# Kernel optimization log

Measured on AMD Instinct MI355X. Metric: run time of the kernel, lower is better.

The kernel has to match this reference:

```python
import jax, jax.numpy as jnp
import numpy as np
import math

BLKQ = 64
BLKK = 32
TOPK_FRAC = 0.1


def setup_inputs() -> dict:
    key = jax.random.key(0)
    k1, k2, k3, k4, k5 = jax.random.split(key, 5)
    B, L, H, D = 1, 8192, 16, 64
    q = jax.random.normal(k1, (B, L, H, D), jnp.float32)
    k = jax.random.normal(k2, (B, L, H, D), jnp.float32)
    v = jax.random.normal(k3, (B, L, H, D), jnp.float32)
    # proj_l initialized with nn.init.normal_ (std=1) in the original
    W_proj = jax.random.normal(k4, (D, D), jnp.float32)
    b_proj = jax.random.normal(k5, (D,), jnp.float32)
    return {"q": q, "k": k, "v": v, "W_proj": W_proj, "b_proj": b_proj}


def reference(q, k, v, W_proj, b_proj):
    B, L, H, D = q.shape
    lcm = BLKQ * BLKK // math.gcd(BLKQ, BLKK)
    L_pad = ((L + lcm - 1) // lcm) * lcm
    pad = L_pad - L
    scale = 1.0 / math.sqrt(D)

    # [B, L, H, D] -> [B, H, L_pad, D], zero padded (fused_transpose_pad)
    qt = jnp.transpose(q, (0, 2, 1, 3))
    kt = jnp.transpose(k, (0, 2, 1, 3))
    vt = jnp.transpose(v, (0, 2, 1, 3))
    if pad:
        pw = ((0, 0), (0, 0), (0, pad), (0, 0))
        qt_p = jnp.pad(qt, pw); kt_p = jnp.pad(kt, pw); vt_p = jnp.pad(vt, pw)
    else:
        qt_p, kt_p, vt_p = qt, kt, vt

    # key smoothing (SAGE): subtract per-(b,h) mean of padded k
    km = kt_p.mean(axis=-2, keepdims=True)          # [B, H, 1, D]
    kc = kt_p - km

    M = L_pad // BLKQ
    N = L_pad // BLKK
    # block pooling for routing scores
    pooled_q = qt_p.reshape(B, H, M, BLKQ, D).mean(axis=3)   # [B,H,M,D]
    pooled_k = kc.reshape(B, H, N, BLKK, D).mean(axis=3)     # [B,H,N,D]
    score = jnp.einsum('bhmd,bhnd->bhmn', pooled_q, pooled_k)

    T = min(N, int(TOPK_FRAC * N))                  # real_topk (static)
    _, idx = jax.lax.top_k(score, T)                # [B,H,M,T]
    lut = jnp.sort(idx, axis=-1)

    # gather selected key/value blocks: [B,H,M,T,BLKK,D]
    kb = kc.reshape(B, H, N, BLKK, D)
    vb = vt_p.reshape(B, H, N, BLKK, D)
    kg = jnp.take_along_axis(kb[:, :, None], lut[..., None, None], axis=3)
    vg = jnp.take_along_axis(vb[:, :, None], lut[..., None, None], axis=3)

    qb = qt_p.reshape(B, H, M, BLKQ, D)
    # block-sparse scores: [B,H,M,BLKQ,T,BLKK]
    s = jnp.einsum('bhmqd,bhmtkd->bhmqtk', qb, kg) * scale
    key_pos = lut[..., None] * BLKK + jnp.arange(BLKK)       # [B,H,M,T,BLKK]
    valid = key_pos < L
    s = jnp.where(valid[:, :, :, None, :, :], s, -jnp.inf)
    s = s.reshape(B, H, M, BLKQ, T * BLKK)
    p = jax.nn.softmax(s, axis=-1)
    o_s = jnp.einsum('bhmqn,bhmnd->bhmqd', p, vg.reshape(B, H, M, T * BLKK, D))
    o_s = o_s.reshape(B, H, L_pad, D)[:, :, :L]              # slice to seq_len

    # linear attention branch (softmax feature map over D)
    q_fm = jax.nn.softmax(qt_p[:, :, :L], axis=-1)
    k_fm = jax.nn.softmax(kt_p[:, :, :L], axis=-1)
    kvsum = jnp.einsum('bhld,bhle->bhde', k_fm, vt)          # [B,H,D,D]
    ksum = k_fm.sum(axis=-2)                                 # [B,H,D]
    denom = jnp.einsum('bhld,bhd->bhl', q_fm, ksum)[..., None] + 1e-6
    o_l = jnp.einsum('bhld,bhde->bhle', q_fm, kvsum) / denom
    o_l = o_l @ W_proj.T + b_proj                            # proj_l

    o = jnp.transpose(o_l + o_s, (0, 2, 1, 3))               # [B,L,H,D]
    return o
```

## Files before the change

### kernel.cpp

```cpp
#include <hip/hip_runtime.h>
#include <math.h>

#define SEQL 8192
#define NH 16
#define HD 1024
#define TSEL 25

#define OFF_KVPART 0
#define OFF_KSUM   262144
#define OFF_ZEND   263168
#define OFF_PK     263168
#define OFF_KWT    525312
#define OFF_KSWZ   558080
#define OFF_LUT    131072

typedef __attribute__((ext_vector_type(8))) short bf16x8;
typedef __attribute__((ext_vector_type(4))) float f32x4;
typedef __attribute__((ext_vector_type(4))) unsigned u32x4;
typedef __attribute__((ext_vector_type(2))) unsigned u32x2;

static __device__ inline short f2bf(float f) {
    union { float f; unsigned u; } c; c.f = f;
    unsigned r = (c.u + 0x7FFFu + ((c.u >> 16) & 1u)) >> 16;
    return (short)r;
}
static __device__ inline bf16x8 cvt8(float4 a, float4 b) {
    bf16x8 r;
    r[0] = f2bf(a.x); r[1] = f2bf(a.y); r[2] = f2bf(a.z); r[3] = f2bf(a.w);
    r[4] = f2bf(b.x); r[5] = f2bf(b.y); r[6] = f2bf(b.z); r[7] = f2bf(b.w);
    return r;
}
static __device__ inline unsigned cvtpk(float a, float b) {
    unsigned r;
    asm("v_cvt_pk_bf16_f32 %0, %1, %2" : "=v"(r) : "v"(a), "v"(b));
    return r;
}
static __device__ inline float exp2a(float x) {
#if __has_builtin(__builtin_amdgcn_exp2f)
    return __builtin_amdgcn_exp2f(x);
#else
    float r; asm("v_exp_f32 %0, %1" : "=v"(r) : "v"(x)); return r;
#endif
}
#if __has_builtin(__builtin_amdgcn_permlane32_swap)
static __device__ inline unsigned xor32v(unsigned x, bool hi) {
    u32x2 r;
    {
        auto t = __builtin_amdgcn_permlane32_swap(x, x, false, false);
        r[0] = t[0]; r[1] = t[1];
    }
    return hi ? r[0] : r[1];
}
static __device__ inline unsigned xor16v(unsigned x, bool hi) {
    u32x2 r;
    {
        auto t = __builtin_amdgcn_permlane16_swap(x, x, false, false);
        r[0] = t[0]; r[1] = t[1];
    }
    return hi ? r[0] : r[1];
}
#else
static __device__ inline unsigned xor32v(unsigned x, bool hi) {
    unsigned a = x, b;
    asm("v_mov_b32 %0, %1" : "=v"(b) : "v"(x));
    asm("v_permlane32_swap_b32 %0, %1" : "+v"(a), "+v"(b));
    return hi ? a : b;
}
static __device__ inline unsigned xor16v(unsigned x, bool hi) {
    unsigned a = x, b;
    asm("v_mov_b32 %0, %1" : "=v"(b) : "v"(x));
    asm("v_permlane16_swap_b32 %0, %1" : "+v"(a), "+v"(b));
    return hi ? a : b;
}
#endif
static __device__ inline void load_lds16(const void* g, void* l) {
    __builtin_amdgcn_global_load_lds((const __attribute__((address_space(1))) unsigned int*)g,
                                     (__attribute__((address_space(3))) unsigned int*)l,
                                     16, 0, 0);
}

__global__ __launch_bounds__(256) void prep_lin(const float* __restrict__ k,
                                                const float* __restrict__ v,
                                                short* __restrict__ kswz,
                                                short* __restrict__ vswz,
                                                float* __restrict__ pk,
                                                float* __restrict__ kvpart,
                                                float* __restrict__ ksum) {
    __shared__ __align__(16) float kf[2][64][68];
    __shared__ __align__(16) float vv[2][64][68];
    __shared__ float pcol[2][2][4][64];
    int b = blockIdx.x;
    int h = b >> 5, sc = b & 31;
    int t = threadIdx.x;
    int lane = t & 63, w = t >> 6;
    int r32 = t >> 3, ch = t & 7;
    int d0 = (lane >> 4) * 4 + w * 16;
    int e0 = (lane & 15) * 4;
    float acc[16];
    #pragma unroll
    for (int i = 0; i < 16; i++) acc[i] = 0.f;
    float ks_acc = 0.f;

    const float* kb_ = k + (size_t)(sc * 256 + r32) * HD + h * 64 + ch * 8;
    const float* vb_ = v + (size_t)(sc * 256 + r32) * HD + h * 64 + ch * 8;
    float4 K0a = *(const float4*)kb_;
    float4 K0b = *(const float4*)(kb_ + 4);
    float4 K1a = *(const float4*)(kb_ + (size_t)32 * HD);
    float4 K1b = *(const float4*)(kb_ + (size_t)32 * HD + 4);
    float4 V0a = *(const float4*)vb_;
    float4 V0b = *(const float4*)(vb_ + 4);
    float4 V1a = *(const float4*)(vb_ + (size_t)32 * HD);
    float4 V1b = *(const float4*)(vb_ + (size_t)32 * HD + 4);

    #pragma unroll
    for (int ph = 0; ph < 4; ph++) {
        int buf = ph & 1;
        int n0 = sc * 8 + ph * 2;
        {
            *(float4*)&vv[buf][r32][ch * 8]          = V0a;
            *(float4*)&vv[buf][r32][ch * 8 + 4]      = V0b;
            *(float4*)&vv[buf][32 + r32][ch * 8]     = V1a;
            *(float4*)&vv[buf][32 + r32][ch * 8 + 4] = V1b;
        }
        {
            int f = r32 * 8 + (ch ^ (r32 & 7));
            *(bf16x8*)(kswz + (size_t)(h * 256 + n0) * 2048 + f * 8)     = cvt8(K0a, K0b);
            *(bf16x8*)(kswz + (size_t)(h * 256 + n0 + 1) * 2048 + f * 8) = cvt8(K1a, K1b);
        }
        {
            float s_[8] = { K0a.x, K0a.y, K0a.z, K0a.w, K0b.x, K0b.y, K0b.z, K0b.w };
            #pragma unroll
            for (int j = 0; j < 8; j++) {
                s_[j] += __shfl_xor(s_[j], 8, 64);
                s_[j] += __shfl_xor(s_[j], 16, 64);
                s_[j] += __shfl_xor(s_[j], 32, 64);
            }
            if (lane < 8) {
                #pragma unroll
                for (int j = 0; j < 8; j++) pcol[buf][0][w][(t & 7) * 8 + j] = s_[j];
            }
            float s1_[8] = { K1a.x, K1a.y, K1a.z, K1a.w, K1b.x, K1b.y, K1b.z, K1b.w };
            #pragma unroll
            for (int j = 0; j < 8; j++) {
                s1_[j] += __shfl_xor(s1_[j], 8, 64);
                s1_[j] += __shfl_xor(s1_[j], 16, 64);
                s1_[j] += __shfl_xor(s1_[j], 32, 64);
            }
            if (lane < 8) {
                #pragma unroll
                for (int j = 0; j < 8; j++) pcol[buf][1][w][(t & 7) * 8 + j] = s1_[j];
            }
        }
        {
            float mx = fmaxf(fmaxf(fmaxf(K0a.x, K0a.y), fmaxf(K0a.z, K0a.w)),
                             fmaxf(fmaxf(K0b.x, K0b.y), fmaxf(K0b.z, K0b.w)));
            mx = fmaxf(mx, __shfl_xor(mx, 1, 64));
            mx = fmaxf(mx, __shfl_xor(mx, 2, 64));
            mx = fmaxf(mx, __shfl_xor(mx, 4, 64));
            float4 Fa, Fb;
            Fa.x = __expf(K0a.x - mx); Fa.y = __expf(K0a.y - mx);
            Fa.z = __expf(K0a.z - mx); Fa.w = __expf(K0a.w - mx);
            Fb.x = __expf(K0b.x - mx); Fb.y = __expf(K0b.y - mx);
            Fb.z = __expf(K0b.z - mx); Fb.w = __expf(K0b.w - mx);
            float sm = (Fa.x + Fa.y + Fa.z + Fa.w) + (Fb.x + Fb.y + Fb.z + Fb.w);
            sm += __shfl_xor(sm, 1, 64);
            sm += __shfl_xor(sm, 2, 64);
            sm += __shfl_xor(sm, 4, 64);
            float inv = 1.f / sm;
            Fa.x *= inv; Fa.y *= inv; Fa.z *= inv; Fa.w *= inv;
            Fb.x *= inv; Fb.y *= inv; Fb.z *= inv; Fb.w *= inv;
            *(float4*)&kf[buf][r32][ch * 8]     = Fa;
            *(float4*)&kf[buf][r32][ch * 8 + 4] = Fb;
        }
        {
            float mx = fmaxf(fmaxf(fmaxf(K1a.x, K1a.y), fmaxf(K1a.z, K1a.w)),
                             fmaxf(fmaxf(K1b.x, K1b.y), fmaxf(K1b.z, K1b.w)));
            mx = fmaxf(mx, __shfl_xor(mx, 1, 64));
            mx = fmaxf(mx, __shfl_xor(mx, 2, 64));
            mx = fmaxf(mx, __shfl_xor(mx, 4, 64));
            float4 Fa, Fb;
            Fa.x = __expf(K1a.x - mx); Fa.y = __expf(K1a.y - mx);
            Fa.z = __expf(K1a.z - mx); Fa.w = __expf(K1a.w - mx);
            Fb.x = __expf(K1b.x - mx); Fb.y = __expf(K1b.y - mx);
            Fb.z = __expf(K1b.z - mx); Fb.w = __expf(K1b.w - mx);
            float sm = (Fa.x + Fa.y + Fa.z + Fa.w) + (Fb.x + Fb.y + Fb.z + Fb.w);
            sm += __shfl_xor(sm, 1, 64);
            sm += __shfl_xor(sm, 2, 64);
            sm += __shfl_xor(sm, 4, 64);
            float inv = 1.f / sm;
            Fa.x *= inv; Fa.y *= inv; Fa.z *= inv; Fa.w *= inv;
            Fb.x *= inv; Fb.y *= inv; Fb.z *= inv; Fb.w *= inv;
            *(float4*)&kf[buf][32 + r32][ch * 8]     = Fa;
            *(float4*)&kf[buf][32 + r32][ch * 8 + 4] = Fb;
        }
        if (ph < 3) {
            const float* kn = kb_ + (size_t)(ph + 1) * 64 * HD;
            const float* vn = vb_ + (size_t)(ph + 1) * 64 * HD;
            K0a = *(const float4*)kn;
            K0b = *(const float4*)(kn + 4);
            K1a = *(const float4*)(kn + (size_t)32 * HD);
            K1b = *(const float4*)(kn + (size_t)32 * HD + 4);
            V0a = *(const float4*)vn;
            V0b = *(const float4*)(vn + 4);
            V1a = *(const float4*)(vn + (size_t)32 * HD);
            V1b = *(const float4*)(vn + (size_t)32 * HD + 4);
        }
        __syncthreads();
        if (t < 128) {
            int s = t >> 6, d = t & 63;
            pk[(size_t)(h * 256 + n0 + s) * 64 + d] =
                (pcol[buf][s][0][d] + pcol[buf][s][1][d] + pcol[buf][s][2][d] + pcol[buf][s][3][d])
                * (1.f / 32.f);
        }
        {
            int c = w, d = lane;
            #pragma unroll
            for (int s = 0; s < 2; s++) {
                bf16x8 val;
                #pragma unroll
                for (int j = 0; j < 8; j++) val[j] = f2bf(vv[buf][s * 32 + c * 8 + j][d]);
                int f = d * 4 + (c ^ ((d >> 1) & 3));
                *(bf16x8*)(vswz + (size_t)(h * 256 + n0 + s) * 2048 + f * 8) = val;
            }
        }
        #pragma unroll 8
        for (int l = 0; l < 64; l++) {
            float4 kd = *(const float4*)&kf[buf][l][d0];
            float4 ve = *(const float4*)&vv[buf][l][e0];
            acc[0]  += kd.x * ve.x; acc[1]  += kd.x * ve.y; acc[2]  += kd.x * ve.z; acc[3]  += kd.x * ve.w;
            acc[4]  += kd.y * ve.x; acc[5]  += kd.y * ve.y; acc[6]  += kd.y * ve.z; acc[7]  += kd.y * ve.w;
            acc[8]  += kd.z * ve.x; acc[9]  += kd.z * ve.y; acc[10] += kd.z * ve.z; acc[11] += kd.z * ve.w;
            acc[12] += kd.w * ve.x; acc[13] += kd.w * ve.y; acc[14] += kd.w * ve.z; acc[15] += kd.w * ve.w;
        }
        if (t < 64) {
            float s = 0.f;
            #pragma unroll 8
            for (int l = 0; l < 64; l++) s += kf[buf][l][t];
            ks_acc += s;
        }
    }
    float* dst = kvpart + ((size_t)(sc & 3) * 16 + h) * 4096;
    #pragma unroll
    for (int i = 0; i < 4; i++)
        #pragma unroll
        for (int j = 0; j < 4; j++)
            atomicAdd(&dst[(d0 + i) * 64 + e0 + j], acc[i * 4 + j]);
    if (t < 64) atomicAdd(&ksum[h * 64 + t], ks_acc);
}

__global__ __launch_bounds__(256) void score_topk(const float* __restrict__ q,
                                                  const float* __restrict__ pk,
                                                  int* __restrict__ lut) {
    __shared__ __align__(16) float pq_s[64];
    __shared__ __align__(16) float s_s[256];
    __shared__ int wcnt[4];
    int b = blockIdx.x;
    int h = b >> 7, m = b & 127;
    int t = threadIdx.x;
    int lane = t & 63, w = t >> 6;
    if (t < 64) {
        const float* base = q + (size_t)m * 64 * HD + h * 64 + t;
        float s = 0.f;
        #pragma unroll 8
        for (int r = 0; r < 64; r++) s += base[(size_t)r * HD];
        pq_s[t] = s * (1.f / 64.f);
    }
    __syncthreads();
    const float* kr = pk + ((size_t)h * 256 + t) * 64;
    double acc = 0.0;
    #pragma unroll 8
    for (int d = 0; d < 64; d++) acc += (double)pq_s[d] * (double)kr[d];
    float sc = (float)acc;
    s_s[t] = sc;
    __syncthreads();
    int cnt = 0;
    float si = sc;
    #pragma unroll 4
    for (int j4 = 0; j4 < 64; j4++) {
        float4 sv = *(const float4*)&s_s[j4 * 4];
        int j = j4 * 4;
        cnt += (sv.x > si) || (sv.x == si && (j + 0) < t);
        cnt += (sv.y > si) || (sv.y == si && (j + 1) < t);
        cnt += (sv.z > si) || (sv.z == si && (j + 2) < t);
        cnt += (sv.w > si) || (sv.w == si && (j + 3) < t);
    }
    bool sel = cnt < TSEL;
    unsigned long long bal = __ballot(sel);
    if (lane == 0) wcnt[w] = __popcll(bal);
    __syncthreads();
    if (sel) {
        int off = __popcll(bal & ((1ull << lane) - 1ull));
        for (int i = 0; i < w; i++) off += wcnt[i];
        lut[(size_t)b * TSEL + off] = t;
    }
}

__global__ __launch_bounds__(256) void kw_mul(const float* __restrict__ kvpart,
                                              const float* __restrict__ W,
                                              short* __restrict__ kwt) {
    __shared__ __align__(16) float kv[16][68];
    __shared__ __align__(16) float wsm[64][68];
    int h = blockIdx.x >> 2, dq = blockIdx.x & 3;
    int t = threadIdx.x;
    for (int i = t; i < 1024; i += 256) {
        int dl = i >> 6, e = i & 63;
        float s = 0.f;
        #pragma unroll
        for (int p = 0; p < 4; p++)
            s += kvpart[((size_t)p * 16 + h) * 4096 + (dq * 16 + dl) * 64 + e];
        kv[dl][e] = s;
    }
    for (int i = t; i < 4096; i += 256) wsm[i >> 6][i & 63] = W[i];
    __syncthreads();
    int lane = t & 63, wi = t >> 6;
    int dl = lane & 15;
    int db = wi * 16 + (lane >> 4) * 4;
    #pragma unroll
    for (int j = 0; j < 4; j++) {
        int dd = db + j;
        float a = 0.f;
        #pragma unroll
        for (int e4 = 0; e4 < 16; e4++) {
            float4 kq = *(const float4*)&kv[dl][e4 * 4];
            float4 wq = *(const float4*)&wsm[dd][e4 * 4];
            a += kq.x * wq.x + kq.y * wq.y + kq.z * wq.z + kq.w * wq.w;
        }
        kwt[(size_t)h * 4096 + dd * 64 + dq * 16 + dl] = f2bf(a);
    }
}

__global__ __launch_bounds__(256) void sparse_attn_mfma(const float* __restrict__ q,
                                                        const short* __restrict__ kswz,
                                                        const short* __restrict__ vswz,
                                                        const int* __restrict__ lut,
                                                        const short* __restrict__ kwt,
                                                        const float* __restrict__ ksum,
                                                        const float* __restrict__ bproj,
                                                        float* __restrict__ out) {
    __shared__ __align__(16) short Kb[3][2048];
    __shared__ __align__(16) short Vb[3][2048];
    __shared__ int lut_s[TSEL];

    int b = blockIdx.x;
    int x = b & 7, jj = b >> 3;
    int h = x * 2 + (jj >> 7);
    int m = jj & 127;
    int t = threadIdx.x;
    int lane = t & 63, w = t >> 6;
    int l15 = lane & 15, quad = lane >> 4;
    const bool b16 = (t & 16) != 0;
    const bool b32 = (t & 32) != 0;
    const bool beq = (b16 == b32);

    if (t < TSEL) lut_s[t] = lut[(size_t)(h * 128 + m) * TSEL + t];
    __syncthreads();

    {
        size_t base = (size_t)(h * 256 + lut_s[0]) * 2048;
        load_lds16(kswz + base + t * 8, &Kb[0][t * 8]);
        load_lds16(vswz + base + t * 8, &Vb[0][t * 8]);
        load_lds16(kwt + (size_t)h * 4096 + t * 8, &Kb[1][t * 8]);
        load_lds16(kwt + (size_t)h * 4096 + 2048 + t * 8, &Vb[1][t * 8]);
    }

    const float* qrow = q + (size_t)(m * 64 + w * 16 + l15) * HD + h * 64;
    float4 x0 = *(const float4*)(qrow + quad * 8);
    float4 x1 = *(const float4*)(qrow + quad * 8 + 4);
    float4 x2 = *(const float4*)(qrow + 32 + quad * 8);
    float4 x3 = *(const float4*)(qrow + 32 + quad * 8 + 4);
    bf16x8 qa[2];
    qa[0] = cvt8(x0, x1);
    qa[1] = cvt8(x2, x3);

    float mx = fmaxf(fmaxf(fmaxf(x0.x, x0.y), fmaxf(x0.z, x0.w)),
                     fmaxf(fmaxf(x1.x, x1.y), fmaxf(x1.z, x1.w)));
    mx = fmaxf(mx, fmaxf(fmaxf(fmaxf(x2.x, x2.y), fmaxf(x2.z, x2.w)),
                         fmaxf(fmaxf(x3.x, x3.y), fmaxf(x3.z, x3.w))));
    mx = fmaxf(mx, __shfl_xor(mx, 16, 64));
    mx = fmaxf(mx, __shfl_xor(mx, 32, 64));
    x0.x = __expf(x0.x - mx); x0.y = __expf(x0.y - mx); x0.z = __expf(x0.z - mx); x0.w = __expf(x0.w - mx);
    x1.x = __expf(x1.x - mx); x1.y = __expf(x1.y - mx); x1.z = __expf(x1.z - mx); x1.w = __expf(x1.w - mx);
    x2.x = __expf(x2.x - mx); x2.y = __expf(x2.y - mx); x2.z = __expf(x2.z - mx); x2.w = __expf(x2.w - mx);
    x3.x = __expf(x3.x - mx); x3.y = __expf(x3.y - mx); x3.z = __expf(x3.z - mx); x3.w = __expf(x3.w - mx);
    float sm = (x0.x + x0.y + x0.z + x0.w) + (x1.x + x1.y + x1.z + x1.w)
             + (x2.x + x2.y + x2.z + x2.w) + (x3.x + x3.y + x3.z + x3.w);
    sm += __shfl_xor(sm, 16, 64);
    sm += __shfl_xor(sm, 32, 64);
    float qsc = 1.f / sm;
    float4 ka0 = *(const float4*)(ksum + h * 64 + quad * 8);
    float4 ka1 = *(const float4*)(ksum + h * 64 + quad * 8 + 4);
    float4 ka2 = *(const float4*)(ksum + h * 64 + 32 + quad * 8);
    float4 ka3 = *(const float4*)(ksum + h * 64 + 32 + quad * 8 + 4);
    float dq = x0.x * ka0.x + x0.y * ka0.y + x0.z * ka0.z + x0.w * ka0.w
             + x1.x * ka1.x + x1.y * ka1.y + x1.z * ka1.z + x1.w * ka1.w
             + x2.x * ka2.x + x2.y * ka2.y + x2.z * ka2.z + x2.w * ka2.w
             + x3.x * ka3.x + x3.y * ka3.y + x3.z * ka3.z + x3.w * ka3.w;
    dq += __shfl_xor(dq, 16, 64);
    dq += __shfl_xor(dq, 32, 64);
    float invd = 1.f / (dq * qsc + 1e-6f);
    x0.x *= qsc; x0.y *= qsc; x0.z *= qsc; x0.w *= qsc;
    x1.x *= qsc; x1.y *= qsc; x1.z *= qsc; x1.w *= qsc;
    x2.x *= qsc; x2.y *= qsc; x2.z *= qsc; x2.w *= qsc;
    x3.x *= qsc; x3.y *= qsc; x3.z *= qsc; x3.w *= qsc;
    bf16x8 qf[2];
    qf[0] = cvt8(x0, x1);
    qf[1] = cvt8(x2, x3);

    __syncthreads();

    f32x4 Ol[4];
    #pragma unroll
    for (int dt = 0; dt < 4; dt++) Ol[dt] = (f32x4){0.f, 0.f, 0.f, 0.f};
    __builtin_amdgcn_s_setprio(1);
    #pragma unroll
    for (int dt = 0; dt < 4; dt++) {
        #pragma unroll
        for (int kc = 0; kc < 2; kc++) {
            int flat = (dt * 16 + l15) * 64 + kc * 32 + quad * 8;
            bf16x8 a = (dt < 2) ? *(const bf16x8*)&Kb[1][flat]
                                : *(const bf16x8*)&Vb[1][flat - 2048];
            Ol[dt] = __builtin_amdgcn_mfma_f32_16x16x32_bf16(a, qf[kc], Ol[dt], 0, 0, 0);
        }
    }
    __builtin_amdgcn_s_setprio(0);

    __syncthreads();
    {
        size_t base = (size_t)(h * 256 + lut_s[1]) * 2048;
        load_lds16(kswz + base + t * 8, &Kb[1][t * 8]);
        load_lds16(vswz + base + t * 8, &Vb[1][t * 8]);
    }

    f32x4 O[4];
    #pragma unroll
    for (int dt = 0; dt < 4; dt++) O[dt] = (f32x4){0.f, 0.f, 0.f, 0.f};
    float l_loc = 0.f;
    const f32x4 z = (f32x4){0.f, 0.f, 0.f, 0.f};
    const float EC = 1.44269504f * 0.125f;

    int bc = 0;
    for (int ti = 0; ti < TSEL; ti++) {
        if (ti > 0) {
            if (ti < TSEL - 1) asm volatile("s_waitcnt vmcnt(2)" ::: "memory");
            else               asm volatile("s_waitcnt vmcnt(0)" ::: "memory");
            __builtin_amdgcn_s_barrier();
            __builtin_amdgcn_sched_barrier(0);
        }
        if (ti + 2 < TSEL) {
            int bs = bc ? bc - 1 : 2;
            size_t base = (size_t)(h * 256 + lut_s[ti + 2]) * 2048;
            load_lds16(kswz + base + t * 8, &Kb[bs][t * 8]);
            load_lds16(vswz + base + t * 8, &Vb[bs][t * 8]);
        }
        int r0 = l15, r1 = 16 + l15;
        bf16x8 a00 = *(const bf16x8*)&Kb[bc][(r0 * 8 + (quad ^ (r0 & 7))) * 8];
        bf16x8 a01 = *(const bf16x8*)&Kb[bc][(r0 * 8 + ((4 + quad) ^ (r0 & 7))) * 8];
        bf16x8 a10 = *(const bf16x8*)&Kb[bc][(r1 * 8 + (quad ^ (r1 & 7))) * 8];
        bf16x8 a11 = *(const bf16x8*)&Kb[bc][(r1 * 8 + ((4 + quad) ^ (r1 & 7))) * 8];
        bf16x8 va[4];
        #pragma unroll
        for (int dt = 0; dt < 4; dt++) {
            int d = dt * 16 + l15;
            va[dt] = *(const bf16x8*)&Vb[bc][(d * 4 + (quad ^ ((d >> 1) & 3))) * 8];
        }
        __builtin_amdgcn_s_setprio(1);
        f32x4 s0 = __builtin_amdgcn_mfma_f32_16x16x32_bf16(a00, qa[0], z, 0, 0, 0);
        s0 = __builtin_amdgcn_mfma_f32_16x16x32_bf16(a01, qa[1], s0, 0, 0, 0);
        f32x4 s1 = __builtin_amdgcn_mfma_f32_16x16x32_bf16(a10, qa[0], z, 0, 0, 0);
        s1 = __builtin_amdgcn_mfma_f32_16x16x32_bf16(a11, qa[1], s1, 0, 0, 0);
        __builtin_amdgcn_s_setprio(0);

        float p0[4], p1[4];
        #pragma unroll
        for (int r = 0; r < 4; r++) {
            p0[r] = exp2a(s0[r] * EC);
            p1[r] = exp2a(s1[r] * EC);
        }
        l_loc += ((p0[0] + p0[1]) + (p0[2] + p0[3])) + ((p1[0] + p1[1]) + (p1[2] + p1[3]));

        unsigned c0 = cvtpk(p0[0], p0[1]);
        unsigned c1 = cvtpk(p0[2], p0[3]);
        unsigned c2 = cvtpk(p1[0], p1[1]);
        unsigned c3 = cvtpk(p1[2], p1[3]);
        unsigned d0_ = xor32v(c0, b32), d1_ = xor32v(c1, b32);
        unsigned d2_ = xor32v(c2, b32), d3_ = xor32v(c3, b32);
        unsigned cc0 = b32 ? c2 : c0,  cc1 = b32 ? c3 : c1;
        unsigned dd0 = b32 ? d2_ : d0_, dd1 = b32 ? d3_ : d1_;
        unsigned sw0 = beq ? cc0 : dd0, sw1 = beq ? cc1 : dd1;
        unsigned t0_ = beq ? dd0 : cc0, t1_ = beq ? dd1 : cc1;
        unsigned rv0 = xor16v(t0_, b16), rv1 = xor16v(t1_, b16);
        u32x4 pw;
        pw[0] = b16 ? rv0 : sw0; pw[1] = b16 ? rv1 : sw1;
        pw[2] = b16 ? sw0 : rv0; pw[3] = b16 ? sw1 : rv1;
        bf16x8 pb = __builtin_bit_cast(bf16x8, pw);

        __builtin_amdgcn_s_setprio(1);
        #pragma unroll
        for (int dt = 0; dt < 4; dt++)
            O[dt] = __builtin_amdgcn_mfma_f32_16x16x32_bf16(va[dt], pb, O[dt], 0, 0, 0);
        __builtin_amdgcn_s_setprio(0);

        bc++; if (bc == 3) bc = 0;
    }

    l_loc += __shfl_xor(l_loc, 16, 64);
    l_loc += __shfl_xor(l_loc, 32, 64);
    float inv = 1.f / l_loc;
    float* dst = out + (size_t)(m * 64 + w * 16 + l15) * HD + h * 64;
    #pragma unroll
    for (int dt = 0; dt < 4; dt++) {
        float4 bv = *(const float4*)(bproj + dt * 16 + quad * 4);
        float4 o;
        o.x = O[dt][0] * inv + Ol[dt][0] * invd + bv.x;
        o.y = O[dt][1] * inv + Ol[dt][1] * invd + bv.y;
        o.z = O[dt][2] * inv + Ol[dt][2] * invd + bv.z;
        o.w = O[dt][3] * inv + Ol[dt][3] * invd + bv.w;
        *(float4*)(dst + dt * 16 + quad * 4) = o;
    }
}

extern "C" void kernel_launch(void* const* d_in, const int* in_sizes, int n_in,
                              void* d_out, int out_size, void* d_ws, size_t ws_size,
                              hipStream_t stream) {
    const float* q  = (const float*)d_in[0];
    const float* k  = (const float*)d_in[1];
    const float* v  = (const float*)d_in[2];
    const float* W  = (const float*)d_in[3];
    const float* bp = (const float*)d_in[4];
    float* out = (float*)d_out;
    float* ws = (float*)d_ws;

    float* kvpart = ws + OFF_KVPART;
    float* ksum   = ws + OFF_KSUM;
    float* pk     = ws + OFF_PK;
    short* kwt    = (short*)(ws + OFF_KWT);
    short* kswz   = (short*)(ws + OFF_KSWZ);
    short* vswz   = kswz + (size_t)16 * 256 * 2048;
    int*   lut    = (int*)(ws + OFF_LUT);

    hipMemsetAsync(ws, 0, OFF_ZEND * sizeof(float), stream);
    prep_lin<<<512, 256, 0, stream>>>(k, v, kswz, vswz, pk, kvpart, ksum);
    kw_mul<<<64, 256, 0, stream>>>(kvpart, W, kwt);
    score_topk<<<2048, 256, 0, stream>>>(q, pk, lut);
    sparse_attn_mfma<<<2048, 256, 0, stream>>>(q, kswz, vswz, lut, kwt, ksum, bp, out);
}
```

Measured before the change: 268.9 us.

## Software-pipeline QK MFMA of the next tile with softmax/PV of the current tile

```diff
diff --git a/kernel.cpp b/kernel.cpp
--- a/kernel.cpp
+++ b/kernel.cpp
@@ -86,9 +86,9 @@
                                                 float* __restrict__ pk,
                                                 float* __restrict__ kvpart,
                                                 float* __restrict__ ksum) {
-    __shared__ __align__(16) float kf[2][64][68];
-    __shared__ __align__(16) float vv[2][64][68];
-    __shared__ float pcol[2][2][4][64];
+    __shared__ __align__(16) float kf[64][68];
+    __shared__ __align__(16) float vv[64][68];
+    __shared__ float pcol[2][4][64];
     int b = blockIdx.x;
     int h = b >> 5, sc = b & 31;
     int t = threadIdx.x;
@@ -114,13 +114,12 @@
 
     #pragma unroll
     for (int ph = 0; ph < 4; ph++) {
-        int buf = ph & 1;
         int n0 = sc * 8 + ph * 2;
         {
-            *(float4*)&vv[buf][r32][ch * 8]          = V0a;
-            *(float4*)&vv[buf][r32][ch * 8 + 4]      = V0b;
-            *(float4*)&vv[buf][32 + r32][ch * 8]     = V1a;
-            *(float4*)&vv[buf][32 + r32][ch * 8 + 4] = V1b;
+            *(float4*)&vv[r32][ch * 8]          = V0a;
+            *(float4*)&vv[r32][ch * 8 + 4]      = V0b;
+            *(float4*)&vv[32 + r32][ch * 8]     = V1a;
+            *(float4*)&vv[32 + r32][ch * 8 + 4] = V1b;
         }
         {
             int f = r32 * 8 + (ch ^ (r32 & 7));
@@ -137,7 +136,7 @@
             }
             if (lane < 8) {
                 #pragma unroll
-                for (int j = 0; j < 8; j++) pcol[buf][0][w][(t & 7) * 8 + j] = s_[j];
+                for (int j = 0; j < 8; j++) pcol[0][w][(t & 7) * 8 + j] = s_[j];
             }
             float s1_[8] = { K1a.x, K1a.y, K1a.z, K1a.w, K1b.x, K1b.y, K1b.z, K1b.w };
             #pragma unroll
@@ -148,7 +147,7 @@
             }
             if (lane < 8) {
                 #pragma unroll
-                for (int j = 0; j < 8; j++) pcol[buf][1][w][(t & 7) * 8 + j] = s1_[j];
+                for (int j = 0; j < 8; j++) pcol[1][w][(t & 7) * 8 + j] = s1_[j];
             }
         }
         {
@@ -169,8 +168,8 @@
             float inv = 1.f / sm;
             Fa.x *= inv; Fa.y *= inv; Fa.z *= inv; Fa.w *= inv;
             Fb.x *= inv; Fb.y *= inv; Fb.z *= inv; Fb.w *= inv;
-            *(float4*)&kf[buf][r32][ch * 8]     = Fa;
-            *(float4*)&kf[buf][r32][ch * 8 + 4] = Fb;
+            *(float4*)&kf[r32][ch * 8]     = Fa;
+            *(float4*)&kf[r32][ch * 8 + 4] = Fb;
         }
         {
             float mx = fmaxf(fmaxf(fmaxf(K1a.x, K1a.y), fmaxf(K1a.z, K1a.w)),
@@ -190,8 +189,8 @@
             float inv = 1.f / sm;
             Fa.x *= inv; Fa.y *= inv; Fa.z *= inv; Fa.w *= inv;
             Fb.x *= inv; Fb.y *= inv; Fb.z *= inv; Fb.w *= inv;
-            *(float4*)&kf[buf][32 + r32][ch * 8]     = Fa;
-            *(float4*)&kf[buf][32 + r32][ch * 8 + 4] = Fb;
+            *(float4*)&kf[32 + r32][ch * 8]     = Fa;
+            *(float4*)&kf[32 + r32][ch * 8 + 4] = Fb;
         }
         if (ph < 3) {
             const float* kn = kb_ + (size_t)(ph + 1) * 64 * HD;
@@ -209,7 +208,7 @@
         if (t < 128) {
             int s = t >> 6, d = t & 63;
             pk[(size_t)(h * 256 + n0 + s) * 64 + d] =
-                (pcol[buf][s][0][d] + pcol[buf][s][1][d] + pcol[buf][s][2][d] + pcol[buf][s][3][d])
+                (pcol[s][0][d] + pcol[s][1][d] + pcol[s][2][d] + pcol[s][3][d])
                 * (1.f / 32.f);
         }
         {
@@ -218,15 +217,15 @@
             for (int s = 0; s < 2; s++) {
                 bf16x8 val;
                 #pragma unroll
-                for (int j = 0; j < 8; j++) val[j] = f2bf(vv[buf][s * 32 + c * 8 + j][d]);
+                for (int j = 0; j < 8; j++) val[j] = f2bf(vv[s * 32 + c * 8 + j][d]);
                 int f = d * 4 + (c ^ ((d >> 1) & 3));
                 *(bf16x8*)(vswz + (size_t)(h * 256 + n0 + s) * 2048 + f * 8) = val;
             }
         }
         #pragma unroll 8
         for (int l = 0; l < 64; l++) {
-            float4 kd = *(const float4*)&kf[buf][l][d0];
-            float4 ve = *(const float4*)&vv[buf][l][e0];
+            float4 kd = *(const float4*)&kf[l][d0];
+            float4 ve = *(const float4*)&vv[l][e0];
             acc[0]  += kd.x * ve.x; acc[1]  += kd.x * ve.y; acc[2]  += kd.x * ve.z; acc[3]  += kd.x * ve.w;
             acc[4]  += kd.y * ve.x; acc[5]  += kd.y * ve.y; acc[6]  += kd.y * ve.z; acc[7]  += kd.y * ve.w;
             acc[8]  += kd.z * ve.x; acc[9]  += kd.z * ve.y; acc[10] += kd.z * ve.z; acc[11] += kd.z * ve.w;
@@ -235,9 +234,10 @@
         if (t < 64) {
             float s = 0.f;
             #pragma unroll 8
-            for (int l = 0; l < 64; l++) s += kf[buf][l][t];
+            for (int l = 0; l < 64; l++) s += kf[l][t];
             ks_acc += s;
         }
+        __syncthreads();
     }
     float* dst = kvpart + ((size_t)(sc & 3) * 16 + h) * 4096;
     #pragma unroll
@@ -438,46 +438,41 @@
     const f32x4 z = (f32x4){0.f, 0.f, 0.f, 0.f};
     const float EC = 1.44269504f * 0.125f;
 
-    int bc = 0;
-    for (int ti = 0; ti < TSEL; ti++) {
-        if (ti > 0) {
-            if (ti < TSEL - 1) asm volatile("s_waitcnt vmcnt(2)" ::: "memory");
-            else               asm volatile("s_waitcnt vmcnt(0)" ::: "memory");
-            __builtin_amdgcn_s_barrier();
-            __builtin_amdgcn_sched_barrier(0);
-        }
-        if (ti + 2 < TSEL) {
-            int bs = bc ? bc - 1 : 2;
-            size_t base = (size_t)(h * 256 + lut_s[ti + 2]) * 2048;
-            load_lds16(kswz + base + t * 8, &Kb[bs][t * 8]);
-            load_lds16(vswz + base + t * 8, &Vb[bs][t * 8]);
-        }
+    auto stage = [&](int ti, int BS) {
+        size_t base = (size_t)(h * 256 + lut_s[ti]) * 2048;
+        load_lds16(kswz + base + t * 8, &Kb[BS][t * 8]);
+        load_lds16(vswz + base + t * 8, &Vb[BS][t * 8]);
+    };
+    auto qk_read = [&](int BC, f32x4& S0, f32x4& S1,
+                       bf16x8& V0, bf16x8& V1, bf16x8& V2, bf16x8& V3) {
         int r0 = l15, r1 = 16 + l15;
-        bf16x8 a00 = *(const bf16x8*)&Kb[bc][(r0 * 8 + (quad ^ (r0 & 7))) * 8];
-        bf16x8 a01 = *(const bf16x8*)&Kb[bc][(r0 * 8 + ((4 + quad) ^ (r0 & 7))) * 8];
-        bf16x8 a10 = *(const bf16x8*)&Kb[bc][(r1 * 8 + (quad ^ (r1 & 7))) * 8];
-        bf16x8 a11 = *(const bf16x8*)&Kb[bc][(r1 * 8 + ((4 + quad) ^ (r1 & 7))) * 8];
-        bf16x8 va[4];
-        #pragma unroll
-        for (int dt = 0; dt < 4; dt++) {
-            int d = dt * 16 + l15;
-            va[dt] = *(const bf16x8*)&Vb[bc][(d * 4 + (quad ^ ((d >> 1) & 3))) * 8];
+        bf16x8 a00 = *(const bf16x8*)&Kb[BC][(r0 * 8 + (quad ^ (r0 & 7))) * 8];
+        bf16x8 a01 = *(const bf16x8*)&Kb[BC][(r0 * 8 + ((4 + quad) ^ (r0 & 7))) * 8];
+        bf16x8 a10 = *(const bf16x8*)&Kb[BC][(r1 * 8 + (quad ^ (r1 & 7))) * 8];
+        bf16x8 a11 = *(const bf16x8*)&Kb[BC][(r1 * 8 + ((4 + quad) ^ (r1 & 7))) * 8];
+        {
+            int d_0 = l15,      d_1 = 16 + l15, d_2 = 32 + l15, d_3 = 48 + l15;
+            V0 = *(const bf16x8*)&Vb[BC][(d_0 * 4 + (quad ^ ((d_0 >> 1) & 3))) * 8];
+            V1 = *(const bf16x8*)&Vb[BC][(d_1 * 4 + (quad ^ ((d_1 >> 1) & 3))) * 8];
+            V2 = *(const bf16x8*)&Vb[BC][(d_2 * 4 + (quad ^ ((d_2 >> 1) & 3))) * 8];
+            V3 = *(const bf16x8*)&Vb[BC][(d_3 * 4 + (quad ^ ((d_3 >> 1) & 3))) * 8];
         }
         __builtin_amdgcn_s_setprio(1);
-        f32x4 s0 = __builtin_amdgcn_mfma_f32_16x16x32_bf16(a00, qa[0], z, 0, 0, 0);
-        s0 = __builtin_amdgcn_mfma_f32_16x16x32_bf16(a01, qa[1], s0, 0, 0, 0);
-        f32x4 s1 = __builtin_amdgcn_mfma_f32_16x16x32_bf16(a10, qa[0], z, 0, 0, 0);
-        s1 = __builtin_amdgcn_mfma_f32_16x16x32_bf16(a11, qa[1], s1, 0, 0, 0);
+        S0 = __builtin_amdgcn_mfma_f32_16x16x32_bf16(a00, qa[0], z, 0, 0, 0);
+        S0 = __builtin_amdgcn_mfma_f32_16x16x32_bf16(a01, qa[1], S0, 0, 0, 0);
+        S1 = __builtin_amdgcn_mfma_f32_16x16x32_bf16(a10, qa[0], z, 0, 0, 0);
+        S1 = __builtin_amdgcn_mfma_f32_16x16x32_bf16(a11, qa[1], S1, 0, 0, 0);
         __builtin_amdgcn_s_setprio(0);
-
+    };
+    auto tail = [&](f32x4 S0, f32x4 S1,
+                    bf16x8 V0, bf16x8 V1, bf16x8 V2, bf16x8 V3) {
         float p0[4], p1[4];
         #pragma unroll
         for (int r = 0; r < 4; r++) {
-            p0[r] = exp2a(s0[r] * EC);
-            p1[r] = exp2a(s1[r] * EC);
+            p0[r] = exp2a(S0[r] * EC);
+            p1[r] = exp2a(S1[r] * EC);
         }
         l_loc += ((p0[0] + p0[1]) + (p0[2] + p0[3])) + ((p1[0] + p1[1]) + (p1[2] + p1[3]));
-
         unsigned c0 = cvtpk(p0[0], p0[1]);
         unsigned c1 = cvtpk(p0[2], p0[3]);
         unsigned c2 = cvtpk(p1[0], p1[1]);
@@ -493,15 +488,48 @@
         pw[0] = b16 ? rv0 : sw0; pw[1] = b16 ? rv1 : sw1;
         pw[2] = b16 ? sw0 : rv0; pw[3] = b16 ? sw1 : rv1;
         bf16x8 pb = __builtin_bit_cast(bf16x8, pw);
-
         __builtin_amdgcn_s_setprio(1);
-        #pragma unroll
-        for (int dt = 0; dt < 4; dt++)
-            O[dt] = __builtin_amdgcn_mfma_f32_16x16x32_bf16(va[dt], pb, O[dt], 0, 0, 0);
+        O[0] = __builtin_amdgcn_mfma_f32_16x16x32_bf16(V0, pb, O[0], 0, 0, 0);
+        O[1] = __builtin_amdgcn_mfma_f32_16x16x32_bf16(V1, pb, O[1], 0, 0, 0);
+        O[2] = __builtin_amdgcn_mfma_f32_16x16x32_bf16(V2, pb, O[2], 0, 0, 0);
+        O[3] = __builtin_amdgcn_mfma_f32_16x16x32_bf16(V3, pb, O[3], 0, 0, 0);
         __builtin_amdgcn_s_setprio(0);
-
+    };
+
+    f32x4 sA0, sA1, sB0, sB1;
+    bf16x8 vA0, vA1, vA2, vA3, vB0, vB1, vB2, vB3;
+
+    stage(2, 2);
+    qk_read(0, sA0, sA1, vA0, vA1, vA2, vA3);
+    int bc = 1;
+    for (int tt = 1; tt < 23; tt += 2) {
+        asm volatile("s_waitcnt vmcnt(2)" ::: "memory");
+        __builtin_amdgcn_s_barrier();
+        __builtin_amdgcn_sched_barrier(0);
+        stage(tt + 2, bc ? bc - 1 : 2);
+        qk_read(bc, sB0, sB1, vB0, vB1, vB2, vB3);
+        tail(sA0, sA1, vA0, vA1, vA2, vA3);
         bc++; if (bc == 3) bc = 0;
-    }
+        asm volatile("s_waitcnt vmcnt(2)" ::: "memory");
+        __builtin_amdgcn_s_barrier();
+        __builtin_amdgcn_sched_barrier(0);
+        stage(tt + 3, bc ? bc - 1 : 2);
+        qk_read(bc, sA0, sA1, vA0, vA1, vA2, vA3);
+        tail(sB0, sB1, vB0, vB1, vB2, vB3);
+        bc++; if (bc == 3) bc = 0;
+    }
+    asm volatile("s_waitcnt vmcnt(2)" ::: "memory");
+    __builtin_amdgcn_s_barrier();
+    __builtin_amdgcn_sched_barrier(0);
+    qk_read(bc, sB0, sB1, vB0, vB1, vB2, vB3);
+    tail(sA0, sA1, vA0, vA1, vA2, vA3);
+    bc++; if (bc == 3) bc = 0;
+    asm volatile("s_waitcnt vmcnt(0)" ::: "memory");
+    __builtin_amdgcn_s_barrier();
+    __builtin_amdgcn_sched_barrier(0);
+    qk_read(bc, sA0, sA1, vA0, vA1, vA2, vA3);
+    tail(sB0, sB1, vB0, vB1, vB2, vB3);
+    tail(sA0, sA1, vA0, vA1, vA2, vA3);
 
     l_loc += __shfl_xor(l_loc, 16, 64);
     l_loc += __shfl_xor(l_loc, 32, 64);
```

After: 276.0 us. 2.6% more time.

## Fuse score/top-k routing into sparse attention kernel and double prep_lin grid

Applied to the files above, without the earlier changes.

```diff
diff --git a/kernel.cpp b/kernel.cpp
--- a/kernel.cpp
+++ b/kernel.cpp
@@ -12,7 +12,6 @@
 #define OFF_PK     263168
 #define OFF_KWT    525312
 #define OFF_KSWZ   558080
-#define OFF_LUT    131072
 
 typedef __attribute__((ext_vector_type(8))) short bf16x8;
 typedef __attribute__((ext_vector_type(4))) float f32x4;
@@ -86,11 +85,11 @@
                                                 float* __restrict__ pk,
                                                 float* __restrict__ kvpart,
                                                 float* __restrict__ ksum) {
-    __shared__ __align__(16) float kf[2][64][68];
-    __shared__ __align__(16) float vv[2][64][68];
-    __shared__ float pcol[2][2][4][64];
+    __shared__ __align__(16) float kf[64][68];
+    __shared__ __align__(16) float vv[64][68];
+    __shared__ float pcol[2][4][64];
     int b = blockIdx.x;
-    int h = b >> 5, sc = b & 31;
+    int h = b >> 6, sc = b & 63;
     int t = threadIdx.x;
     int lane = t & 63, w = t >> 6;
     int r32 = t >> 3, ch = t & 7;
@@ -101,8 +100,8 @@
     for (int i = 0; i < 16; i++) acc[i] = 0.f;
     float ks_acc = 0.f;
 
-    const float* kb_ = k + (size_t)(sc * 256 + r32) * HD + h * 64 + ch * 8;
-    const float* vb_ = v + (size_t)(sc * 256 + r32) * HD + h * 64 + ch * 8;
+    const float* kb_ = k + (size_t)(sc * 128 + r32) * HD + h * 64 + ch * 8;
+    const float* vb_ = v + (size_t)(sc * 128 + r32) * HD + h * 64 + ch * 8;
     float4 K0a = *(const float4*)kb_;
     float4 K0b = *(const float4*)(kb_ + 4);
     float4 K1a = *(const float4*)(kb_ + (size_t)32 * HD);
@@ -113,14 +112,13 @@
     float4 V1b = *(const float4*)(vb_ + (size_t)32 * HD + 4);
 
     #pragma unroll
-    for (int ph = 0; ph < 4; ph++) {
-        int buf = ph & 1;
-        int n0 = sc * 8 + ph * 2;
+    for (int ph = 0; ph < 2; ph++) {
+        int n0 = sc * 4 + ph * 2;
         {
-            *(float4*)&vv[buf][r32][ch * 8]          = V0a;
-            *(float4*)&vv[buf][r32][ch * 8 + 4]      = V0b;
-            *(float4*)&vv[buf][32 + r32][ch * 8]     = V1a;
-            *(float4*)&vv[buf][32 + r32][ch * 8 + 4] = V1b;
+            *(float4*)&vv[r32][ch * 8]          = V0a;
+            *(float4*)&vv[r32][ch * 8 + 4]      = V0b;
+            *(float4*)&vv[32 + r32][ch * 8]     = V1a;
+            *(float4*)&vv[32 + r32][ch * 8 + 4] = V1b;
         }
         {
             int f = r32 * 8 + (ch ^ (r32 & 7));
@@ -137,7 +135,7 @@
             }
             if (lane < 8) {
                 #pragma unroll
-                for (int j = 0; j < 8; j++) pcol[buf][0][w][(t & 7) * 8 + j] = s_[j];
+                for (int j = 0; j < 8; j++) pcol[0][w][(t & 7) * 8 + j] = s_[j];
             }
             float s1_[8] = { K1a.x, K1a.y, K1a.z, K1a.w, K1b.x, K1b.y, K1b.z, K1b.w };
             #pragma unroll
@@ -148,7 +146,7 @@
             }
             if (lane < 8) {
                 #pragma unroll
-                for (int j = 0; j < 8; j++) pcol[buf][1][w][(t & 7) * 8 + j] = s1_[j];
+                for (int j = 0; j < 8; j++) pcol[1][w][(t & 7) * 8 + j] = s1_[j];
             }
         }
         {
@@ -169,8 +167,8 @@
             float inv = 1.f / sm;
             Fa.x *= inv; Fa.y *= inv; Fa.z *= inv; Fa.w *= inv;
             Fb.x *= inv; Fb.y *= inv; Fb.z *= inv; Fb.w *= inv;
-            *(float4*)&kf[buf][r32][ch * 8]     = Fa;
-            *(float4*)&kf[buf][r32][ch * 8 + 4] = Fb;
+            *(float4*)&kf[r32][ch * 8]     = Fa;
+            *(float4*)&kf[r32][ch * 8 + 4] = Fb;
         }
         {
             float mx = fmaxf(fmaxf(fmaxf(K1a.x, K1a.y), fmaxf(K1a.z, K1a.w)),
@@ -190,12 +188,12 @@
             float inv = 1.f / sm;
             Fa.x *= inv; Fa.y *= inv; Fa.z *= inv; Fa.w *= inv;
             Fb.x *= inv; Fb.y *= inv; Fb.z *= inv; Fb.w *= inv;
-            *(float4*)&kf[buf][32 + r32][ch * 8]     = Fa;
-            *(float4*)&kf[buf][32 + r32][ch * 8 + 4] = Fb;
-        }
-        if (ph < 3) {
-            const float* kn = kb_ + (size_t)(ph + 1) * 64 * HD;
-            const float* vn = vb_ + (size_t)(ph + 1) * 64 * HD;
+            *(float4*)&kf[32 + r32][ch * 8]     = Fa;
+            *(float4*)&kf[32 + r32][ch * 8 + 4] = Fb;
+        }
+        if (ph < 1) {
+            const float* kn = kb_ + (size_t)64 * HD;
+            const float* vn = vb_ + (size_t)64 * HD;
             K0a = *(const float4*)kn;
             K0b = *(const float4*)(kn + 4);
             K1a = *(const float4*)(kn + (size_t)32 * HD);
@@ -209,7 +207,7 @@
         if (t < 128) {
             int s = t >> 6, d = t & 63;
             pk[(size_t)(h * 256 + n0 + s) * 64 + d] =
-                (pcol[buf][s][0][d] + pcol[buf][s][1][d] + pcol[buf][s][2][d] + pcol[buf][s][3][d])
+                (pcol[s][0][d] + pcol[s][1][d] + pcol[s][2][d] + pcol[s][3][d])
                 * (1.f / 32.f);
         }
         {
@@ -218,15 +216,15 @@
             for (int s = 0; s < 2; s++) {
                 bf16x8 val;
                 #pragma unroll
-                for (int j = 0; j < 8; j++) val[j] = f2bf(vv[buf][s * 32 + c * 8 + j][d]);
+                for (int j = 0; j < 8; j++) val[j] = f2bf(vv[s * 32 + c * 8 + j][d]);
                 int f = d * 4 + (c ^ ((d >> 1) & 3));
                 *(bf16x8*)(vswz + (size_t)(h * 256 + n0 + s) * 2048 + f * 8) = val;
             }
         }
         #pragma unroll 8
         for (int l = 0; l < 64; l++) {
-            float4 kd = *(const float4*)&kf[buf][l][d0];
-            float4 ve = *(const float4*)&vv[buf][l][e0];
+            float4 kd = *(const float4*)&kf[l][d0];
+            float4 ve = *(const float4*)&vv[l][e0];
             acc[0]  += kd.x * ve.x; acc[1]  += kd.x * ve.y; acc[2]  += kd.x * ve.z; acc[3]  += kd.x * ve.w;
             acc[4]  += kd.y * ve.x; acc[5]  += kd.y * ve.y; acc[6]  += kd.y * ve.z; acc[7]  += kd.y * ve.w;
             acc[8]  += kd.z * ve.x; acc[9]  += kd.z * ve.y; acc[10] += kd.z * ve.z; acc[11] += kd.z * ve.w;
@@ -235,9 +233,10 @@
         if (t < 64) {
             float s = 0.f;
             #pragma unroll 8
-            for (int l = 0; l < 64; l++) s += kf[buf][l][t];
+            for (int l = 0; l < 64; l++) s += kf[l][t];
             ks_acc += s;
         }
+        __syncthreads();
     }
     float* dst = kvpart + ((size_t)(sc & 3) * 16 + h) * 4096;
     #pragma unroll
@@ -246,53 +245,6 @@
         for (int j = 0; j < 4; j++)
             atomicAdd(&dst[(d0 + i) * 64 + e0 + j], acc[i * 4 + j]);
     if (t < 64) atomicAdd(&ksum[h * 64 + t], ks_acc);
-}
-
-__global__ __launch_bounds__(256) void score_topk(const float* __restrict__ q,
-                                                  const float* __restrict__ pk,
-                                                  int* __restrict__ lut) {
-    __shared__ __align__(16) float pq_s[64];
-    __shared__ __align__(16) float s_s[256];
-    __shared__ int wcnt[4];
-    int b = blockIdx.x;
-    int h = b >> 7, m = b & 127;
-    int t = threadIdx.x;
-    int lane = t & 63, w = t >> 6;
-    if (t < 64) {
-        const float* base = q + (size_t)m * 64 * HD + h * 64 + t;
-        float s = 0.f;
-        #pragma unroll 8
-        for (int r = 0; r < 64; r++) s += base[(size_t)r * HD];
-        pq_s[t] = s * (1.f / 64.f);
-    }
-    __syncthreads();
-    const float* kr = pk + ((size_t)h * 256 + t) * 64;
-    double acc = 0.0;
-    #pragma unroll 8
-    for (int d = 0; d < 64; d++) acc += (double)pq_s[d] * (double)kr[d];
-    float sc = (float)acc;
-    s_s[t] = sc;
-    __syncthreads();
-    int cnt = 0;
-    float si = sc;
-    #pragma unroll 4
-    for (int j4 = 0; j4 < 64; j4++) {
-        float4 sv = *(const float4*)&s_s[j4 * 4];
-        int j = j4 * 4;
-        cnt += (sv.x > si) || (sv.x == si && (j + 0) < t);
-        cnt += (sv.y > si) || (sv.y == si && (j + 1) < t);
-        cnt += (sv.z > si) || (sv.z == si && (j + 2) < t);
-        cnt += (sv.w > si) || (sv.w == si && (j + 3) < t);
-    }
-    bool sel = cnt < TSEL;
-    unsigned long long bal = __ballot(sel);
-    if (lane == 0) wcnt[w] = __popcll(bal);
-    __syncthreads();
-    if (sel) {
-        int off = __popcll(bal & ((1ull << lane) - 1ull));
-        for (int i = 0; i < w; i++) off += wcnt[i];
-        lut[(size_t)b * TSEL + off] = t;
-    }
 }
 
 __global__ __launch_bounds__(256) void kw_mul(const float* __restrict__ kvpart,
@@ -332,13 +284,16 @@
 __global__ __launch_bounds__(256) void sparse_attn_mfma(const float* __restrict__ q,
                                                         const short* __restrict__ kswz,
                                                         const short* __restrict__ vswz,
-                                                        const int* __restrict__ lut,
+                                                        const float* __restrict__ pk,
                                                         const short* __restrict__ kwt,
                                                         const float* __restrict__ ksum,
                                                         const float* __restrict__ bproj,
                                                         float* __restrict__ out) {
     __shared__ __align__(16) short Kb[3][2048];
     __shared__ __align__(16) short Vb[3][2048];
+    __shared__ __align__(16) float pq_s[64];
+    __shared__ __align__(16) float s_s[256];
+    __shared__ int wcnt[4];
     __shared__ int lut_s[TSEL];
 
     int b = blockIdx.x;
@@ -352,15 +307,54 @@
     const bool b32 = (t & 32) != 0;
     const bool beq = (b16 == b32);
 
-    if (t < TSEL) lut_s[t] = lut[(size_t)(h * 128 + m) * TSEL + t];
+    {
+        load_lds16(kwt + (size_t)h * 4096 + t * 8, &Kb[1][t * 8]);
+        load_lds16(kwt + (size_t)h * 4096 + 2048 + t * 8, &Vb[1][t * 8]);
+    }
+
+    if (t < 64) {
+        const float* base = q + (size_t)m * 64 * HD + h * 64 + t;
+        float s = 0.f;
+        #pragma unroll 8
+        for (int r = 0; r < 64; r++) s += base[(size_t)r * HD];
+        pq_s[t] = s * (1.f / 64.f);
+    }
     __syncthreads();
+    {
+        const float* kr = pk + ((size_t)h * 256 + t) * 64;
+        double acc = 0.0;
+        #pragma unroll 8
+        for (int d = 0; d < 64; d++) acc += (double)pq_s[d] * (double)kr[d];
+        float sc_ = (float)acc;
+        s_s[t] = sc_;
+        __syncthreads();
+        int cnt = 0;
+        float si = sc_;
+        #pragma unroll 4
+        for (int j4 = 0; j4 < 64; j4++) {
+            float4 sv = *(const float4*)&s_s[j4 * 4];
+            int j = j4 * 4;
+            cnt += (sv.x > si) || (sv.x == si && (j + 0) < t);
+            cnt += (sv.y > si) || (sv.y == si && (j + 1) < t);
+            cnt += (sv.z > si) || (sv.z == si && (j + 2) < t);
+            cnt += (sv.w > si) || (sv.w == si && (j + 3) < t);
+        }
+        bool sel = cnt < TSEL;
+        unsigned long long bal = __ballot(sel);
+        if (lane == 0) wcnt[w] = __popcll(bal);
+        __syncthreads();
+        if (sel) {
+            int off = __popcll(bal & ((1ull << lane) - 1ull));
+            for (int i = 0; i < w; i++) off += wcnt[i];
+            lut_s[off] = t;
+        }
+        __syncthreads();
+    }
 
     {
         size_t base = (size_t)(h * 256 + lut_s[0]) * 2048;
         load_lds16(kswz + base + t * 8, &Kb[0][t * 8]);
         load_lds16(vswz + base + t * 8, &Vb[0][t * 8]);
-        load_lds16(kwt + (size_t)h * 4096 + t * 8, &Kb[1][t * 8]);
-        load_lds16(kwt + (size_t)h * 4096 + 2048 + t * 8, &Vb[1][t * 8]);
     }
 
     const float* qrow = q + (size_t)(m * 64 + w * 16 + l15) * HD + h * 64;
@@ -536,11 +530,9 @@
     short* kwt    = (short*)(ws + OFF_KWT);
     short* kswz   = (short*)(ws + OFF_KSWZ);
     short* vswz   = kswz + (size_t)16 * 256 * 2048;
-    int*   lut    = (int*)(ws + OFF_LUT);
 
     hipMemsetAsync(ws, 0, OFF_ZEND * sizeof(float), stream);
-    prep_lin<<<512, 256, 0, stream>>>(k, v, kswz, vswz, pk, kvpart, ksum);
+    prep_lin<<<1024, 256, 0, stream>>>(k, v, kswz, vswz, pk, kvpart, ksum);
     kw_mul<<<64, 256, 0, stream>>>(kvpart, W, kwt);
-    score_topk<<<2048, 256, 0, stream>>>(q, pk, lut);
-    sparse_attn_mfma<<<2048, 256, 0, stream>>>(q, kswz, vswz, lut, kwt, ksum, bp, out);
-}
+    sparse_attn_mfma<<<2048, 256, 0, stream>>>(q, kswz, vswz, pk, kwt, ksum, bp, out);
+}
```

After: 294.8 us. +9.6%, slower.
